# Kernel tuning notes

Measured on AMD Instinct MI355X. Metric: run time of the kernel, lower is better.

The kernel has to match this reference:

```python
import jax, jax.numpy as jnp
import numpy as np
from jax import lax

K_KNN = 20           # DGCNN default neighborhood size
SLOPE = 0.2          # LeakyReLU negative slope


def _leaky(x):
    return jnp.where(x >= 0, x, SLOPE * x)


def _knn(x, k):
    # x: [B, N, C] -> idx [B, N, k] of nearest neighbors (incl. self) in feature space
    xx = jnp.sum(x * x, axis=-1)                       # [B, N]
    d = xx[:, :, None] + xx[:, None, :] - 2.0 * jnp.einsum('bnc,bmc->bnm', x, x)
    return lax.top_k(-d, k)[1]                          # [B, N, k]


def _edge_conv(x, idx, w, b):
    # x: [B, N, C]; idx: [B, N, k]; w: [O, 2C]; b: [O]
    neigh = jax.vmap(lambda xt, i: xt[i])(x, idx)       # [B, N, k, C]
    center = jnp.broadcast_to(x[:, :, None, :], neigh.shape)
    feat = jnp.concatenate([neigh - center, center], axis=-1)  # [B, N, k, 2C]
    h = _leaky(jnp.einsum('bnkc,oc->bnko', feat, w) + b)
    return jnp.max(h, axis=2)                           # [B, N, O]


def setup_inputs() -> dict:
    key = jax.random.key(0)
    ks = jax.random.split(key, 20)
    B, N, J, KR = 4, 4096, 24, 4
    layers = [64, 128, 256]

    def w_init(k, o, i):
        return jax.random.normal(k, (o, i), jnp.float32) / np.sqrt(i)

    inp = {
        'V': jax.random.normal(ks[0], (B, N, 3), jnp.float32),
        'W': jax.random.uniform(ks[1], (B, J, N), jnp.float32),
        'skeletonOneRingIdx': jax.random.randint(ks[2], (B, J, KR), 0, J),
    }
    # geoNet edge-conv params (input channels per layer: 3, 64, 128 -> 2C inputs)
    inp['g1_w'] = w_init(ks[3], 64, 6);    inp['g1_b'] = jnp.zeros((64,), jnp.float32)
    inp['g2_w'] = w_init(ks[4], 128, 128); inp['g2_b'] = jnp.zeros((128,), jnp.float32)
    inp['g3_w'] = w_init(ks[5], 256, 256); inp['g3_b'] = jnp.zeros((256,), jnp.float32)
    # skeleton edge-conv params (inputs: 451 -> 902, 256 -> 512, 128 -> 256)
    inp['s1_w'] = w_init(ks[6], 256, 902); inp['s1_b'] = jnp.zeros((256,), jnp.float32)
    inp['s2_w'] = w_init(ks[7], 128, 512); inp['s2_b'] = jnp.zeros((128,), jnp.float32)
    inp['s3_w'] = w_init(ks[8], 64, 256);  inp['s3_b'] = jnp.zeros((64,), jnp.float32)
    # jointMLP 1x1 convs: 448 -> 512 -> 256 -> 3
    inp['m1_w'] = w_init(ks[9], 512, 448);  inp['m1_b'] = jnp.zeros((512,), jnp.float32)
    inp['m2_w'] = w_init(ks[10], 256, 512); inp['m2_b'] = jnp.zeros((256,), jnp.float32)
    inp['m3_w'] = w_init(ks[11], 3, 256);   inp['m3_b'] = jnp.zeros((3,), jnp.float32)
    return inp


def reference(V, W, skeletonOneRingIdx,
              g1_w, g1_b, g2_w, g2_b, g3_w, g3_b,
              s1_w, s1_b, s2_w, s2_b, s3_w, s3_b,
              m1_w, m1_b, m2_w, m2_b, m3_w, m3_b):
    # ---- geoNet: DGCNN with dynamic kNN, output cat([xyz, l1, l2, l3]) -> [B, N, 451]
    outs = [V]
    h = V
    for w, b in ((g1_w, g1_b), (g2_w, g2_b), (g3_w, g3_b)):
        idx = _knn(h, K_KNN)
        h = _edge_conv(h, idx, w, b)
        outs.append(h)
    feat = jnp.concatenate(outs, axis=-1)                # [B, N, 451]

    # ---- weighted pooling onto skeleton joints
    pooled = jnp.einsum('bjn,bnc->bjc', W, feat)
    pooled = pooled / (jnp.sum(W, axis=-1, keepdims=True) + 1e-5)  # [B, J, 451]

    # ---- skeleton edge convs with fixed one-ring idx
    v1 = _edge_conv(pooled, skeletonOneRingIdx, s1_w, s1_b)  # [B, J, 256]
    v2 = _edge_conv(v1, skeletonOneRingIdx, s2_w, s2_b)      # [B, J, 128]
    v3 = _edge_conv(v2, skeletonOneRingIdx, s3_w, s3_b)      # [B, J, 64]

    joints = jnp.concatenate([v1, v2, v3], axis=-1)          # [B, J, 448]
    h = _leaky(jnp.einsum('bjc,oc->bjo', joints, m1_w) + m1_b)
    h = _leaky(jnp.einsum('bjc,oc->bjo', h, m2_w) + m2_b)
    out = jnp.einsum('bjc,oc->bjo', h, m3_w) + m3_b          # [B, J, 3]
    return out
```

## Files before the change

kernel.cpp:

```cpp
#include <hip/hip_runtime.h>
#include <hip/hip_bf16.h>
#include <float.h>

#define B_   4
#define N_   4096
#define J_   24
#define KR_  4
#define KNN_ 20
#define SLOPE 0.2f
#define SLABN 64
#define NSLAB (N_ / SLABN)
#define NTILE 32
#define SCAP 768
#define KSLACK 8u

typedef __attribute__((ext_vector_type(8))) short bf16x8;
typedef __attribute__((ext_vector_type(4))) float f32x4;

__global__ void k_norm(const float* __restrict__ h, float* __restrict__ xx, int C) {
    int i = blockIdx.x * blockDim.x + threadIdx.x;
    if (i >= B_ * N_) return;
    const float* hp = h + (size_t)i * C;
    float s = 0.f;
    for (int c = 0; c < C; ++c) { float v = hp[c]; s += v * v; }
    xx[i] = s;
}

__device__ __forceinline__ unsigned mapf(float f) {
    unsigned u = __float_as_uint(f);
    return (u & 0x80000000u) ? ~u : (u | 0x80000000u);
}
__device__ __forceinline__ unsigned key16(float f) {
    return mapf(f) >> 16;
}

__global__ void k_split(const float* __restrict__ h, unsigned short* __restrict__ hi,
                        unsigned short* __restrict__ lo, int total4) {
    int i = blockIdx.x * 256 + threadIdx.x;
    if (i >= total4) return;
    float4 v = ((const float4*)h)[i];
    ushort4 h4, l4;
    {
        unsigned u = __float_as_uint(v.x); h4.x = (unsigned short)(u >> 16);
        float r = v.x - __uint_as_float(u & 0xffff0000u); l4.x = (unsigned short)(__float_as_uint(r) >> 16);
    }
    {
        unsigned u = __float_as_uint(v.y); h4.y = (unsigned short)(u >> 16);
        float r = v.y - __uint_as_float(u & 0xffff0000u); l4.y = (unsigned short)(__float_as_uint(r) >> 16);
    }
    {
        unsigned u = __float_as_uint(v.z); h4.z = (unsigned short)(u >> 16);
        float r = v.z - __uint_as_float(u & 0xffff0000u); l4.z = (unsigned short)(__float_as_uint(r) >> 16);
    }
    {
        unsigned u = __float_as_uint(v.w); h4.w = (unsigned short)(u >> 16);
        float r = v.w - __uint_as_float(u & 0xffff0000u); l4.w = (unsigned short)(__float_as_uint(r) >> 16);
    }
    ((ushort4*)hi)[i] = h4;
    ((ushort4*)lo)[i] = l4;
}

__global__ __launch_bounds__(256) void k_dist(const unsigned short* __restrict__ Hi,
                                              const unsigned short* __restrict__ Lo,
                                              int C,
                                              const float* __restrict__ xxall,
                                              unsigned short* __restrict__ Dall, int b0) {
    __shared__ unsigned short tile[128][136];
    int b = b0 + blockIdx.y;
    const unsigned short* XH = Hi + (size_t)b * N_ * C;
    const unsigned short* XL = Lo + (size_t)b * N_ * C;
    const float* xxb = xxall + (size_t)b * N_;
    unsigned short* D = Dall + (size_t)blockIdx.y * N_ * N_;

    int t = blockIdx.x;
    int ti = 0;
    while (t >= NTILE - ti) { t -= NTILE - ti; ++ti; }
    int tj = ti + t;
    int row0 = ti * 128, col0 = tj * 128;
    int tid  = threadIdx.x;
    int wv   = tid >> 6, lane = tid & 63;
    int wr   = wv >> 1,  wc   = wv & 1;
    int rbase = row0 + wr * 64;
    int cbase = col0 + wc * 64;
    int lp    = lane & 15;
    int kgrp  = lane >> 4;

    f32x4 acc[4][4];
#pragma unroll
    for (int i = 0; i < 4; ++i)
#pragma unroll
        for (int j = 0; j < 4; ++j) acc[i][j] = (f32x4){0.f, 0.f, 0.f, 0.f};

    for (int ks = 0; ks < C; ks += 32) {
        int kb = ks + kgrp * 8;
        bf16x8 ah[4], al[4];
#pragma unroll
        for (int fi = 0; fi < 4; ++fi) {
            size_t ro = (size_t)(rbase + fi * 16 + lp) * C + kb;
            ah[fi] = *(const bf16x8*)(XH + ro);
            al[fi] = *(const bf16x8*)(XL + ro);
        }
#pragma unroll
        for (int fj = 0; fj < 4; ++fj) {
            size_t co = (size_t)(cbase + fj * 16 + lp) * C + kb;
            bf16x8 bh = *(const bf16x8*)(XH + co);
            bf16x8 bl = *(const bf16x8*)(XL + co);
#pragma unroll
            for (int fi = 0; fi < 4; ++fi) {
                acc[fi][fj] = __builtin_amdgcn_mfma_f32_16x16x32_bf16(ah[fi], bh, acc[fi][fj], 0, 0, 0);
                acc[fi][fj] = __builtin_amdgcn_mfma_f32_16x16x32_bf16(ah[fi], bl, acc[fi][fj], 0, 0, 0);
                acc[fi][fj] = __builtin_amdgcn_mfma_f32_16x16x32_bf16(al[fi], bh, acc[fi][fj], 0, 0, 0);
            }
        }
    }

    float xxrv = xxb[rbase + lane];
    float xxcv = xxb[cbase + lane];
    int rsub = (lane >> 4) * 4;
#pragma unroll
    for (int fi = 0; fi < 4; ++fi) {
#pragma unroll
        for (int fj = 0; fj < 4; ++fj) {
            float xc = __shfl(xxcv, fj * 16 + lp, 64);
#pragma unroll
            for (int r = 0; r < 4; ++r) {
                float xr = __shfl(xxrv, fi * 16 + rsub + r, 64);
                float d = xr + xc - 2.f * acc[fi][fj][r];
                tile[wr * 64 + fi * 16 + rsub + r][wc * 64 + fj * 16 + lp] =
                    (unsigned short)key16(d);
            }
        }
    }
    __syncthreads();

    {
        int r0   = tid >> 4;
        int cseg = (tid & 15) * 8;
#pragma unroll
        for (int q = 0; q < 8; ++q) {
            int row = r0 + q * 16;
            *(uint4*)(D + (size_t)(row0 + row) * N_ + col0 + cseg) =
                *(const uint4*)&tile[row][cseg];
        }
    }
    if (ti == tj) return;
    {
        int c0g = tid >> 4;
        int g   = tid & 15;
#pragma unroll
        for (int cq = 0; cq < 8; ++cq) {
            int c = c0g + cq * 16;
            unsigned short s[8];
#pragma unroll
            for (int q = 0; q < 8; ++q) s[q] = tile[g * 8 + q][c];
            *(uint4*)(D + (size_t)(col0 + c) * N_ + row0 + g * 8) = *(const uint4*)s;
        }
    }
}

__device__ __forceinline__ unsigned long long shflx64(unsigned long long v, int m) {
    unsigned lo = (unsigned)v, hi = (unsigned)(v >> 32);
    lo = (unsigned)__shfl_xor((int)lo, m, 64);
    hi = (unsigned)__shfl_xor((int)hi, m, 64);
    return ((unsigned long long)hi << 32) | lo;
}

__device__ __forceinline__ float bsort64f(float v, int lane) {
#pragma unroll
    for (int k = 2; k <= 64; k <<= 1) {
#pragma unroll
        for (int j = k >> 1; j > 0; j >>= 1) {
            float o = __shfl_xor(v, j, 64);
            bool keepmin = (((lane & j) == 0) == ((lane & k) == 0));
            float mn = fminf(v, o), mx = fmaxf(v, o);
            v = keepmin ? mn : mx;
        }
    }
    return v;
}

__device__ __forceinline__ unsigned bsort64i(unsigned v, int lane) {
#pragma unroll
    for (int k = 2; k <= 64; k <<= 1) {
#pragma unroll
        for (int j = k >> 1; j > 0; j >>= 1) {
            unsigned o = (unsigned)__shfl_xor((int)v, j, 64);
            bool keepmin = (((lane & j) == 0) == ((lane & k) == 0));
            unsigned mn = (v < o) ? v : o;
            unsigned mx = (v < o) ? o : v;
            v = keepmin ? mn : mx;
        }
    }
    return v;
}

__device__ __forceinline__ unsigned long long bsort64u(unsigned long long v, int lane) {
#pragma unroll
    for (int k = 2; k <= 64; k <<= 1) {
#pragma unroll
        for (int j = k >> 1; j > 0; j >>= 1) {
            unsigned long long o = shflx64(v, j);
            bool keepmin = (((lane & j) == 0) == ((lane & k) == 0));
            bool oless = o < v;
            unsigned long long mn = oless ? o : v;
            unsigned long long mx = oless ? v : o;
            v = keepmin ? mn : mx;
        }
    }
    return v;
}

__global__ __launch_bounds__(256) void k_sel(const unsigned short* __restrict__ Dall,
                                             const float* __restrict__ Xall, int C,
                                             const float* __restrict__ xxall,
                                             int* __restrict__ knnIdx, int b0) {
    __shared__ unsigned sidx[SCAP];
    __shared__ unsigned long long skey[SCAP];
    __shared__ float qf[128];
    __shared__ unsigned stau[4];
    __shared__ int scnt;
    int b = b0 + blockIdx.y;
    const unsigned short* Db = Dall + (size_t)blockIdx.y * N_ * N_;
    const float* Xb  = Xall + (size_t)b * N_ * C;
    const float* xxb = xxall + (size_t)b * N_;
    int* idxout = knnIdx + (size_t)b * N_ * KNN_;
    int ql   = blockIdx.x;
    int wv   = threadIdx.x >> 6;
    int lane = threadIdx.x & 63;
    int gbase = wv * 1024 + lane * 16;
    if (threadIdx.x == 0) scnt = 0;
    for (int c = threadIdx.x; c < C; c += 256) qf[c] = Xb[(size_t)ql * C + c];

    const uint4* kp = (const uint4*)(Db + (size_t)ql * N_ + gbase);
    uint4 pa = kp[0], pb = kp[1];
    unsigned kv[16];
    kv[0] = pa.x & 0xffffu;  kv[1] = pa.x >> 16;
    kv[2] = pa.y & 0xffffu;  kv[3] = pa.y >> 16;
    kv[4] = pa.z & 0xffffu;  kv[5] = pa.z >> 16;
    kv[6] = pa.w & 0xffffu;  kv[7] = pa.w >> 16;
    kv[8] = pb.x & 0xffffu;  kv[9] = pb.x >> 16;
    kv[10] = pb.y & 0xffffu; kv[11] = pb.y >> 16;
    kv[12] = pb.z & 0xffffu; kv[13] = pb.z >> 16;
    kv[14] = pb.w & 0xffffu; kv[15] = pb.w >> 16;

    unsigned mn = kv[0];
#pragma unroll
    for (int t = 1; t < 16; ++t) mn = (kv[t] < mn) ? kv[t] : mn;
    mn = bsort64i(mn, lane);
    unsigned tw = (unsigned)__shfl((int)mn, 19, 64);
    if (lane == 0) stau[wv] = tw;
    __syncthreads();
    unsigned tau = stau[0];
    tau = (stau[1] < tau) ? stau[1] : tau;
    tau = (stau[2] < tau) ? stau[2] : tau;
    tau = (stau[3] < tau) ? stau[3] : tau;
    tau += KSLACK;
    if (tau > 0xffffu) tau = 0xffffu;

#pragma unroll
    for (int t = 0; t < 16; ++t) {
        if (kv[t] <= tau) {
            int p = atomicAdd(&scnt, 1);
            if (p < SCAP) sidx[p] = (unsigned)(gbase + t);
        }
    }
    __syncthreads();
    int S = scnt; if (S > SCAP) S = SCAP;
    float xxq = xxb[ql];
    const float4* xq4 = (const float4*)qf;
    for (int s = threadIdx.x; s < S; s += 256) {
        int j = (int)sidx[s];
        const float4* xj = (const float4*)(Xb + (size_t)j * C);
        float a0 = 0.f, a1 = 0.f, a2 = 0.f, a3 = 0.f;
        for (int c4 = 0; c4 < (C >> 2); ++c4) {
            float4 x = xj[c4]; float4 qv = xq4[c4];
            a0 = fmaf(qv.x, x.x, a0);
            a1 = fmaf(qv.y, x.y, a1);
            a2 = fmaf(qv.z, x.z, a2);
            a3 = fmaf(qv.w, x.w, a3);
        }
        float dot = (a0 + a1) + (a2 + a3);
        float d = xxq + xxb[j] - 2.f * dot;
        skey[s] = ((unsigned long long)mapf(d) << 32) | (unsigned)j;
    }
    __syncthreads();
    if (wv != 0) return;
    unsigned long long key = (lane < S) ? skey[lane] : ~0ull;
    key = bsort64u(key, lane);
    for (int consumed = 64; consumed < S; consumed += 44) {
        if (lane >= 20) {
            int src = consumed + lane - 20;
            key = (src < S) ? skey[src] : ~0ull;
        }
        key = bsort64u(key, lane);
    }
    if (lane < KNN_) idxout[ql * KNN_ + lane] = (int)(unsigned)key;
}

__global__ __launch_bounds__(256) void k_selC3(const float* __restrict__ V,
                                               const float* __restrict__ xx,
                                               int* __restrict__ knnIdx) {
    __shared__ unsigned long long sbuf[SCAP];
    __shared__ float stau[4];
    __shared__ int scnt;
    int b    = blockIdx.y;
    const float* Xb  = V + (size_t)b * N_ * 3;
    const float* xxb = xx + (size_t)b * N_;
    int* idxout = knnIdx + (size_t)b * N_ * KNN_;
    int q    = blockIdx.x;
    int wv   = threadIdx.x >> 6;
    int lane = threadIdx.x & 63;
    int gbase = wv * 1024 + lane * 16;
    if (threadIdx.x == 0) scnt = 0;

    float qx = Xb[q * 3], qy = Xb[q * 3 + 1], qz = Xb[q * 3 + 2];
    float xxq = xxb[q];

    float pts[48];
    const float4* src = (const float4*)(Xb + (size_t)gbase * 3);
#pragma unroll
    for (int t = 0; t < 12; ++t) ((float4*)pts)[t] = src[t];

    float dv[16];
#pragma unroll
    for (int t = 0; t < 16; ++t) {
        float dot = qx * pts[3 * t];
        dot = fmaf(qy, pts[3 * t + 1], dot);
        dot = fmaf(qz, pts[3 * t + 2], dot);
        dv[t] = xxq + xxb[gbase + t] - 2.f * dot;
    }

    float mn = dv[0];
#pragma unroll
    for (int t = 1; t < 16; ++t) mn = fminf(mn, dv[t]);
    mn = bsort64f(mn, lane);
    float tw = __shfl(mn, 19, 64);
    if (lane == 0) stau[wv] = tw;
    __syncthreads();
    float tau = fminf(fminf(stau[0], stau[1]), fminf(stau[2], stau[3]));

#pragma unroll
    for (int t = 0; t < 16; ++t) {
        if (dv[t] <= tau) {
            int p = atomicAdd(&scnt, 1);
            if (p < SCAP)
                sbuf[p] = ((unsigned long long)mapf(dv[t]) << 32) | (unsigned)(gbase + t);
        }
    }
    __syncthreads();
    if (wv != 0) return;
    int S = scnt; if (S > SCAP) S = SCAP;
    unsigned long long key = (lane < S) ? sbuf[lane] : ~0ull;
    key = bsort64u(key, lane);
    for (int consumed = 64; consumed < S; consumed += 44) {
        if (lane >= 20) {
            int srci = consumed + lane - 20;
            key = (srci < S) ? sbuf[srci] : ~0ull;
        }
        key = bsort64u(key, lane);
    }
    if (lane < KNN_) idxout[q * KNN_ + lane] = (int)(unsigned)key;
}

__device__ __forceinline__ void prepP_elem(const float* __restrict__ w,
                                           const float* __restrict__ bias,
                                           int C, int O, float* __restrict__ P,
                                           float* __restrict__ b2, int i) {
    int O2 = 2 * O;
    if (i < O2) b2[i] = (i < O) ? 0.f : bias[i - O];
    if (i >= C * O2) return;
    int k = i / O2, col = i % O2;
    float v;
    if (col < O) v = w[(size_t)col * 2 * C + k];
    else { int o = col - O; v = w[(size_t)o * 2 * C + C + k] - w[(size_t)o * 2 * C + k]; }
    P[i] = v;
}
__device__ __forceinline__ void transp_elem(const float* __restrict__ w, int O, int K,
                                            float* __restrict__ wT, int i) {
    if (i >= O * K) return;
    int k = i / O, o = i % O;
    wT[i] = w[(size_t)o * K + k];
}

__global__ void k_prepall(const float* g1w, const float* g1b,
                          const float* g2w, const float* g2b,
                          const float* g3w, const float* g3b,
                          const float* s1w, const float* s1b,
                          const float* s2w, const float* s2b,
                          const float* s3w, const float* s3b,
                          const float* m1w, const float* m2w, const float* m3w,
                          float* P1, float* P2, float* P3, float* P4, float* P5,
                          float* P6, float* P7, float* P8, float* P9,
                          float* bb1, float* bb2, float* bb3,
                          float* bb4, float* bb5, float* bb6) {
    int i = blockIdx.x * 256 + threadIdx.x;
    switch (blockIdx.y) {
        case 0: prepP_elem(g1w, g1b, 3,   64,  P1, bb1, i); break;
        case 1: prepP_elem(g2w, g2b, 64,  128, P2, bb2, i); break;
        case 2: prepP_elem(g3w, g3b, 128, 256, P3, bb3, i); break;
        case 3: prepP_elem(s1w, s1b, 451, 256, P4, bb4, i); break;
        case 4: prepP_elem(s2w, s2b, 256, 128, P5, bb5, i); break;
        case 5: prepP_elem(s3w, s3b, 128, 64,  P6, bb6, i); break;
        case 6: transp_elem(m1w, 512, 448, P7, i); break;
        case 7: transp_elem(m2w, 256, 512, P8, i); break;
        case 8: transp_elem(m3w, 3,   256, P9, i); break;
    }
}

__global__ __launch_bounds__(256) void k_gemm(const float* __restrict__ A, int lda,
                                              const float* __restrict__ Bm,
                                              float* __restrict__ Cm, int ldc,
                                              int M, int N, int K,
                                              const float* __restrict__ bias, int leaky) {
    __shared__ float As[16][68];
    __shared__ float Bs[16][68];
    int tid = threadIdx.x;
    int row0 = blockIdx.y * 64, col0 = blockIdx.x * 64;
    int tr = tid >> 4, tc = tid & 15;
    float acc[4][4] = {{0.f}};
    for (int kt = 0; kt < K; kt += 16) {
#pragma unroll
        for (int i = 0; i < 4; ++i) {
            int e = tid + 256 * i;
            int r = e >> 4, kk = e & 15;
            int gr = row0 + r, gk = kt + kk;
            float v = 0.f;
            if (gr < M && gk < K) v = A[(size_t)gr * lda + gk];
            As[kk][r] = v;
        }
#pragma unroll
        for (int i = 0; i < 4; ++i) {
            int e = tid + 256 * i;
            int kk = e >> 6, c = e & 63;
            int gk = kt + kk, gc = col0 + c;
            float v = 0.f;
            if (gk < K && gc < N) v = Bm[(size_t)gk * N + gc];
            Bs[kk][c] = v;
        }
        __syncthreads();
#pragma unroll
        for (int kk = 0; kk < 16; ++kk) {
            float a[4], bv[4];
            *(float4*)&a[0]  = *(const float4*)&As[kk][tr * 4];
            *(float4*)&bv[0] = *(const float4*)&Bs[kk][tc * 4];
#pragma unroll
            for (int i = 0; i < 4; ++i)
#pragma unroll
                for (int j = 0; j < 4; ++j) acc[i][j] += a[i] * bv[j];
        }
        __syncthreads();
    }
#pragma unroll
    for (int i = 0; i < 4; ++i) {
        int r = row0 + tr * 4 + i;
        if (r >= M) continue;
#pragma unroll
        for (int j = 0; j < 4; ++j) {
            int c = col0 + tc * 4 + j;
            if (c >= N) continue;
            float v = acc[i][j];
            if (bias) v += bias[c];
            if (leaky) v = v >= 0.f ? v : SLOPE * v;
            Cm[(size_t)r * ldc + c] = v;
        }
    }
}

__global__ __launch_bounds__(256) void k_sgemm(const float* __restrict__ A, int lda,
                                               const float* __restrict__ Bm,
                                               float* __restrict__ Cm, int ldc,
                                               int N, int K,
                                               const float* __restrict__ bias, int leaky) {
    extern __shared__ float Arow[];
    int r   = blockIdx.x;
    int c0  = blockIdx.y * 256;
    int tid = threadIdx.x;
    for (int k = tid; k < K; k += 256) Arow[k] = A[(size_t)r * lda + k];
    __syncthreads();
    int c = c0 + tid;
    if (c >= N) return;
    float acc = bias ? bias[c] : 0.f;
    for (int k = 0; k < K; ++k) acc += Arow[k] * Bm[(size_t)k * N + c];
    if (leaky) acc = acc >= 0.f ? acc : SLOPE * acc;
    Cm[(size_t)r * ldc + c] = acc;
}

__global__ void k_gathermax(const float* __restrict__ Y, int O, int R,
                            const int* __restrict__ idx, int kc,
                            float* __restrict__ out, int ldo, int ooff,
                            float* __restrict__ xxout) {
    extern __shared__ int sidx[];
    __shared__ float red[256];
    int br = blockIdx.x;
    int b  = br / R;
    int o  = threadIdx.x;
    if (o < kc) sidx[o] = idx[(size_t)br * kc + o];
    __syncthreads();
    int O2 = 2 * O;
    float z = Y[(size_t)br * O2 + O + o];
    float best = -FLT_MAX;
    for (int k = 0; k < kc; ++k) {
        int m = sidx[k];
        best = fmaxf(best, Y[(size_t)(b * R + m) * O2 + o]);
    }
    float r = z + best;
    r = r >= 0.f ? r : SLOPE * r;
    out[(size_t)br * ldo + ooff + o] = r;
    if (xxout) {
        red[o] = r * r;
        __syncthreads();
        for (int s = blockDim.x >> 1; s > 0; s >>= 1) {
            if (o < s) red[o] += red[o + s];
            __syncthreads();
        }
        if (o == 0) xxout[br] = red[0];
    }
}

__device__ __forceinline__ void chan_map(int b, int c,
                                         const float* Vf, const float* l1,
                                         const float* l2, const float* l3,
                                         const float*& p, int& st) {
    if (c < 3)        { st = 3;   p = Vf + (size_t)b * N_ * 3   + c; }
    else if (c < 67)  { st = 64;  p = l1 + (size_t)b * N_ * 64  + (c - 3); }
    else if (c < 195) { st = 128; p = l2 + (size_t)b * N_ * 128 + (c - 67); }
    else              { st = 256; p = l3 + (size_t)b * N_ * 256 + (c - 195); }
}

__global__ __launch_bounds__(256) void k_pool2(const float* __restrict__ Vf,
                                               const float* __restrict__ l1,
                                               const float* __restrict__ l2,
                                               const float* __restrict__ l3,
                                               const float* __restrict__ W,
                                               float* __restrict__ ppool,
                                               float* __restrict__ psw) {
    __shared__ float Wl[SLABN][J_];
    int blk  = blockIdx.x;
    int b    = blk / NSLAB, slab = blk % NSLAB;
    int n0   = slab * SLABN;
    int tid  = threadIdx.x;

    for (int e = tid; e < J_ * SLABN; e += 256) {
        int j = e / SLABN, n = e % SLABN;
        Wl[n][j] = W[((size_t)b * J_ + j) * N_ + n0 + n];
    }
    __syncthreads();

    if (tid < J_) {
        float s = 0.f;
        for (int n = 0; n < SLABN; ++n) s += Wl[n][tid];
        psw[(size_t)blk * J_ + tid] = s;
    }

    int c0 = tid, c1 = tid + 256;
    const float *p0, *p1 = nullptr; int s0, s1 = 0;
    chan_map(b, c0, Vf, l1, l2, l3, p0, s0);
    bool has1 = (c1 < 451);
    if (has1) chan_map(b, c1, Vf, l1, l2, l3, p1, s1);

    float acc0[J_], acc1[J_];
#pragma unroll
    for (int j = 0; j < J_; ++j) { acc0[j] = 0.f; acc1[j] = 0.f; }

    for (int n = 0; n < SLABN; ++n) {
        float v0 = p0[(size_t)(n0 + n) * s0];
        float v1 = has1 ? p1[(size_t)(n0 + n) * s1] : 0.f;
        const float* wn = &Wl[n][0];
#pragma unroll
        for (int q = 0; q < J_ / 4; ++q) {
            float4 w4 = *(const float4*)(wn + 4 * q);
            acc0[4*q+0] += w4.x * v0;  acc1[4*q+0] += w4.x * v1;
            acc0[4*q+1] += w4.y * v0;  acc1[4*q+1] += w4.y * v1;
            acc0[4*q+2] += w4.z * v0;  acc1[4*q+2] += w4.z * v1;
            acc0[4*q+3] += w4.w * v0;  acc1[4*q+3] += w4.w * v1;
        }
    }
    float* pp = ppool + (size_t)blk * J_ * 451;
#pragma unroll
    for (int j = 0; j < J_; ++j) {
        pp[(size_t)j * 451 + c0] = acc0[j];
        if (has1) pp[(size_t)j * 451 + c1] = acc1[j];
    }
}

__global__ __launch_bounds__(256) void k_poolred(const float* __restrict__ ppool,
                                                 const float* __restrict__ psw,
                                                 float* __restrict__ pooled) {
    int bj = blockIdx.x;
    int b  = bj / J_, j = bj % J_;
    int tid = threadIdx.x;

    float sw = 0.f;
    for (int sl = 0; sl < NSLAB; ++sl) sw += psw[(size_t)(b * NSLAB + sl) * J_ + j];
    float inv = 1.f / (sw + 1e-5f);

    for (int c = tid; c < 451; c += 256) {
        float s = 0.f;
        for (int sl = 0; sl < NSLAB; ++sl)
            s += ppool[((size_t)(b * NSLAB + sl) * J_ + j) * 451 + c];
        pooled[(size_t)bj * 451 + c] = s * inv;
    }
}

extern "C" void kernel_launch(void* const* d_in, const int* in_sizes, int n_in,
                              void* d_out, int out_size, void* d_ws, size_t ws_size,
                              hipStream_t stream) {
    const float* V  = (const float*)d_in[0];
    const float* W  = (const float*)d_in[1];
    const int* ringIdx = (const int*)d_in[2];
    const float* g1w = (const float*)d_in[3];
    const float* g1b = (const float*)d_in[4];
    const float* g2w = (const float*)d_in[5];
    const float* g2b = (const float*)d_in[6];
    const float* g3w = (const float*)d_in[7];
    const float* g3b = (const float*)d_in[8];
    const float* s1w = (const float*)d_in[9];
    const float* s1b = (const float*)d_in[10];
    const float* s2w = (const float*)d_in[11];
    const float* s2b = (const float*)d_in[12];
    const float* s3w = (const float*)d_in[13];
    const float* s3b = (const float*)d_in[14];
    const float* m1w = (const float*)d_in[15];
    const float* m1b = (const float*)d_in[16];
    const float* m2w = (const float*)d_in[17];
    const float* m2b = (const float*)d_in[18];
    const float* m3w = (const float*)d_in[19];
    const float* m3b = (const float*)d_in[20];
    (void)n_in; (void)in_sizes; (void)out_size;

    const int szP1 = 3 * 128,    szP2 = 64 * 256,  szP3 = 128 * 512;
    const int szP4 = 451 * 512,  szP5 = 256 * 256, szP6 = 128 * 128;
    const int szP7 = 448 * 512,  szP8 = 512 * 256, szP9 = 256 * 3;

    auto dreg_floats = [&](int nd) -> size_t {
        size_t a = (size_t)nd * ((size_t)N_ * N_ / 2);
        size_t ymax = (size_t)B_ * N_ * 512;
        size_t pool = (size_t)B_ * NSLAB * J_ * 451 + (size_t)B_ * NSLAB * J_;
        size_t r = a;
        if (ymax > r) r = ymax;
        if (pool > r) r = pool;
        return r;
    };
    auto layout_bytes = [&](int nd) -> size_t {
        size_t f = 0;
        f += (size_t)B_ * N_ * 64 + (size_t)B_ * N_ * 128 + (size_t)B_ * N_ * 256;
        f += (size_t)B_ * N_;
        f += dreg_floats(nd);
        f += 2 * ((size_t)B_ * N_ * 128 / 2);
        f += (size_t)B_ * N_ * KNN_;
        f += (size_t)B_ * J_ * 451 + (size_t)B_ * J_ * 448;
        f += (size_t)B_ * J_ * 512 + (size_t)B_ * J_ * 256;
        f += (size_t)(szP1 + szP2 + szP3 + szP4 + szP5 + szP6 + szP7 + szP8 + szP9);
        f += 128 + 256 + 512 + 512 + 256 + 128;
        return f * 4;
    };
    int nb = 1;
    if (ws_size >= layout_bytes(4)) nb = 4;
    else if (ws_size >= layout_bytes(2)) nb = 2;

    float* ws = (float*)d_ws;
    size_t off = 0;
    float* l1 = ws + off; off += (size_t)B_ * N_ * 64;
    float* l2 = ws + off; off += (size_t)B_ * N_ * 128;
    float* l3 = ws + off; off += (size_t)B_ * N_ * 256;
    float* xx = ws + off; off += (size_t)B_ * N_;
    float* D  = ws + off; off += dreg_floats(nb);
    unsigned short* Dk = (unsigned short*)D;
    float* Y  = D;
    float* ppool = D;
    float* psw   = D + (size_t)B_ * NSLAB * J_ * 451;
    unsigned short* Xhi = (unsigned short*)(ws + off); off += (size_t)B_ * N_ * 128 / 2;
    unsigned short* Xlo = (unsigned short*)(ws + off); off += (size_t)B_ * N_ * 128 / 2;
    int* knnIdx = (int*)(ws + off); off += (size_t)B_ * N_ * KNN_;
    float* pooled = ws + off; off += (size_t)B_ * J_ * 451;
    float* joints = ws + off; off += (size_t)B_ * J_ * 448;
    float* h1 = ws + off; off += (size_t)B_ * J_ * 512;
    float* h2 = ws + off; off += (size_t)B_ * J_ * 256;
    float* P1 = ws + off; off += szP1;
    float* P2 = ws + off; off += szP2;
    float* P3 = ws + off; off += szP3;
    float* P4 = ws + off; off += szP4;
    float* P5 = ws + off; off += szP5;
    float* P6 = ws + off; off += szP6;
    float* P7 = ws + off; off += szP7;
    float* P8 = ws + off; off += szP8;
    float* P9 = ws + off; off += szP9;
    float* bb1 = ws + off; off += 128;
    float* bb2 = ws + off; off += 256;
    float* bb3 = ws + off; off += 512;
    float* bb4 = ws + off; off += 512;
    float* bb5 = ws + off; off += 256;
    float* bb6 = ws + off; off += 128;

    const int M = B_ * N_;
    const int MJ = B_ * J_;
    const int NUTRI = NTILE * (NTILE + 1) / 2;

    k_prepall<<<dim3((szP4 + 255) / 256, 9), 256, 0, stream>>>(
        g1w, g1b, g2w, g2b, g3w, g3b, s1w, s1b, s2w, s2b, s3w, s3b,
        m1w, m2w, m3w, P1, P2, P3, P4, P5, P6, P7, P8, P9,
        bb1, bb2, bb3, bb4, bb5, bb6);

    k_norm<<<(M + 255) / 256, 256, 0, stream>>>(V, xx, 3);
    k_selC3<<<dim3(N_, B_), 256, 0, stream>>>(V, xx, knnIdx);
    k_gemm<<<dim3(2, M / 64), 256, 0, stream>>>(V, 3, P1, Y, 128, M, 128, 3, bb1, 0);
    k_gathermax<<<M, 64, KNN_ * sizeof(int), stream>>>(Y, 64, N_, knnIdx, KNN_, l1, 64, 0, xx);

    k_split<<<(M * 64 / 4 + 255) / 256, 256, 0, stream>>>(l1, Xhi, Xlo, M * 64 / 4);
    for (int g = 0; g < B_; g += nb) {
        k_dist<<<dim3(NUTRI, nb), 256, 0, stream>>>(Xhi, Xlo, 64, xx, Dk, g);
        k_sel<<<dim3(N_, nb), 256, 0, stream>>>(Dk, l1, 64, xx, knnIdx, g);
    }
    k_gemm<<<dim3(4, M / 64), 256, 0, stream>>>(l1, 64, P2, Y, 256, M, 256, 64, bb2, 0);
    k_gathermax<<<M, 128, KNN_ * sizeof(int), stream>>>(Y, 128, N_, knnIdx, KNN_, l2, 128, 0, xx);

    k_split<<<(M * 128 / 4 + 255) / 256, 256, 0, stream>>>(l2, Xhi, Xlo, M * 128 / 4);
    for (int g = 0; g < B_; g += nb) {
        k_dist<<<dim3(NUTRI, nb), 256, 0, stream>>>(Xhi, Xlo, 128, xx, Dk, g);
        k_sel<<<dim3(N_, nb), 256, 0, stream>>>(Dk, l2, 128, xx, knnIdx, g);
    }
    k_gemm<<<dim3(8, M / 64), 256, 0, stream>>>(l2, 128, P3, Y, 512, M, 512, 128, bb3, 0);
    k_gathermax<<<M, 256, KNN_ * sizeof(int), stream>>>(Y, 256, N_, knnIdx, KNN_, l3, 256, 0, nullptr);

    k_pool2<<<B_ * NSLAB, 256, 0, stream>>>(V, l1, l2, l3, W, ppool, psw);
    k_poolred<<<MJ, 256, 0, stream>>>(ppool, psw, pooled);

    k_sgemm<<<dim3(MJ, 2), 256, 451 * sizeof(float), stream>>>(pooled, 451, P4, Y, 512, 512, 451, bb4, 0);
    k_gathermax<<<MJ, 256, KR_ * sizeof(int), stream>>>(Y, 256, J_, ringIdx, KR_, joints, 448, 0, nullptr);

    k_sgemm<<<dim3(MJ, 1), 256, 256 * sizeof(float), stream>>>(joints, 448, P5, Y, 256, 256, 256, bb5, 0);
    k_gathermax<<<MJ, 128, KR_ * sizeof(int), stream>>>(Y, 128, J_, ringIdx, KR_, joints, 448, 256, nullptr);

    k_sgemm<<<dim3(MJ, 1), 256, 128 * sizeof(float), stream>>>(joints + 256, 448, P6, Y, 128, 128, 128, bb6, 0);
    k_gathermax<<<MJ, 64, KR_ * sizeof(int), stream>>>(Y, 64, J_, ringIdx, KR_, joints, 448, 384, nullptr);

    k_sgemm<<<dim3(MJ, 2), 256, 448 * sizeof(float), stream>>>(joints, 448, P7, h1, 512, 512, 448, m1b, 1);
    k_sgemm<<<dim3(MJ, 1), 256, 512 * sizeof(float), stream>>>(h1, 512, P8, h2, 256, 256, 512, m2b, 1);
    k_sgemm<<<dim3(MJ, 1), 256, 256 * sizeof(float), stream>>>(h2, 256, P9, (float*)d_out, 3, 3, 256, m3b, 0);
}
```

Before: 890.5 us.

## Replace bitonic-sort kNN selection with ballot-based radix select

Swaps the full 64-lane bitonic sorts used to find the per-wave threshold and the final top-20 for a ballot/popcount radix-select. The threshold now needs one ballot per key bit instead of 21 shuffle/compare stages. The final merge keeps only the current winners and refills the rest of the wave from the candidate buffer, then ranks the winners with a small shared-memory count. The aim is to cut shuffle and sort work in the selection kernels. The trade-off is more serial ballot loops (32 plus 12 bits per round) and extra subtle tie-handling logic, since only the low 12 index bits are used.

Result: slower. 961.1 us (+7.9%).

```diff
diff --git a/kernel.cpp b/kernel.cpp
--- a/kernel.cpp
+++ b/kernel.cpp
@@ -158,56 +158,69 @@
     }
 }
 
-__device__ __forceinline__ unsigned long long shflx64(unsigned long long v, int m) {
-    unsigned lo = (unsigned)v, hi = (unsigned)(v >> 32);
-    lo = (unsigned)__shfl_xor((int)lo, m, 64);
-    hi = (unsigned)__shfl_xor((int)hi, m, 64);
-    return ((unsigned long long)hi << 32) | lo;
-}
-
-__device__ __forceinline__ float bsort64f(float v, int lane) {
-#pragma unroll
-    for (int k = 2; k <= 64; k <<= 1) {
-#pragma unroll
-        for (int j = k >> 1; j > 0; j >>= 1) {
-            float o = __shfl_xor(v, j, 64);
-            bool keepmin = (((lane & j) == 0) == ((lane & k) == 0));
-            float mn = fminf(v, o), mx = fmaxf(v, o);
-            v = keepmin ? mn : mx;
-        }
-    }
-    return v;
-}
-
-__device__ __forceinline__ unsigned bsort64i(unsigned v, int lane) {
-#pragma unroll
-    for (int k = 2; k <= 64; k <<= 1) {
-#pragma unroll
-        for (int j = k >> 1; j > 0; j >>= 1) {
-            unsigned o = (unsigned)__shfl_xor((int)v, j, 64);
-            bool keepmin = (((lane & j) == 0) == ((lane & k) == 0));
-            unsigned mn = (v < o) ? v : o;
-            unsigned mx = (v < o) ? o : v;
-            v = keepmin ? mn : mx;
-        }
-    }
-    return v;
-}
-
-__device__ __forceinline__ unsigned long long bsort64u(unsigned long long v, int lane) {
-#pragma unroll
-    for (int k = 2; k <= 64; k <<= 1) {
-#pragma unroll
-        for (int j = k >> 1; j > 0; j >>= 1) {
-            unsigned long long o = shflx64(v, j);
-            bool keepmin = (((lane & j) == 0) == ((lane & k) == 0));
-            bool oless = o < v;
-            unsigned long long mn = oless ? o : v;
-            unsigned long long mx = oless ? v : o;
-            v = keepmin ? mn : mx;
-        }
-    }
-    return v;
+__device__ __forceinline__ unsigned radixsel_wave(unsigned val, int r, int nbits) {
+    unsigned long long cand = ~0ull;
+    unsigned prefix = 0;
+    for (int bit = nbits - 1; bit >= 0; --bit) {
+        unsigned long long z = cand & __ballot(!((val >> bit) & 1u));
+        int cz = __popcll(z);
+        if (cz >= r) cand = z;
+        else { r -= cz; cand &= ~z; prefix |= 1u << bit; }
+    }
+    return prefix;
+}
+
+__device__ __forceinline__ bool top20_round(unsigned long long key, bool active) {
+    unsigned hi = (unsigned)(key >> 32);
+    unsigned lo = (unsigned)key;
+    unsigned long long amask = __ballot(active);
+    int navail = __popcll(amask);
+    if (navail <= KNN_) return active;
+    int r = KNN_;
+    unsigned long long cand = amask;
+    unsigned prefix = 0;
+    for (int bit = 31; bit >= 0; --bit) {
+        unsigned long long z = cand & __ballot(!((hi >> bit) & 1u));
+        int cz = __popcll(z);
+        if (cz >= r) cand = z;
+        else { r -= cz; cand &= ~z; prefix |= 1u << bit; }
+    }
+    unsigned long long c2 = __ballot(active && hi == prefix);
+    unsigned p2 = 0;
+    for (int bit = 11; bit >= 0; --bit) {
+        unsigned long long z = c2 & __ballot(!((lo >> bit) & 1u));
+        int cz = __popcll(z);
+        if (cz >= r) c2 = z;
+        else { r -= cz; c2 &= ~z; p2 |= 1u << bit; }
+    }
+    return active && (hi < prefix || (hi == prefix && lo <= p2));
+}
+
+__device__ __forceinline__ void final_top20(const unsigned long long* skey, int S,
+                                            unsigned long long* wbuf,
+                                            int lane, int* idxout, int obase) {
+    unsigned long long key = (lane < S) ? skey[lane] : ~0ull;
+    bool active = (lane < S) && (lane < 64);
+    int consumed = (S < 64) ? S : 64;
+    int nw = 0;
+    for (;;) {
+        bool win = top20_round(key, active);
+        unsigned long long wb = __ballot(win);
+        nw = __popcll(wb);
+        int pos = __popcll(wb & ((1ull << lane) - 1ull));
+        if (win) wbuf[pos] = key;
+        if (consumed >= S) break;
+        int src = consumed + lane - nw;
+        key = (lane < nw) ? wbuf[lane] : ((src < S) ? skey[src] : ~0ull);
+        active = (lane < nw) || (src >= consumed && src < S);
+        consumed += 64 - nw;
+    }
+    if (lane < nw) {
+        unsigned long long mine = wbuf[lane];
+        int rank = 0;
+        for (int i = 0; i < nw; ++i) rank += (wbuf[i] < mine);
+        idxout[obase + rank] = (int)(unsigned)mine;
+    }
 }
 
 __global__ __launch_bounds__(256) void k_sel(const unsigned short* __restrict__ Dall,
@@ -216,6 +229,7 @@
                                              int* __restrict__ knnIdx, int b0) {
     __shared__ unsigned sidx[SCAP];
     __shared__ unsigned long long skey[SCAP];
+    __shared__ unsigned long long wbuf[24];
     __shared__ float qf[128];
     __shared__ unsigned stau[4];
     __shared__ int scnt;
@@ -225,11 +239,12 @@
     const float* xxb = xxall + (size_t)b * N_;
     int* idxout = knnIdx + (size_t)b * N_ * KNN_;
     int ql   = blockIdx.x;
-    int wv   = threadIdx.x >> 6;
-    int lane = threadIdx.x & 63;
+    int tid  = threadIdx.x;
+    int wv   = tid >> 6;
+    int lane = tid & 63;
     int gbase = wv * 1024 + lane * 16;
-    if (threadIdx.x == 0) scnt = 0;
-    for (int c = threadIdx.x; c < C; c += 256) qf[c] = Xb[(size_t)ql * C + c];
+    if (tid == 0) scnt = 0;
+    for (int c = tid; c < C; c += 256) qf[c] = Xb[(size_t)ql * C + c];
 
     const uint4* kp = (const uint4*)(Db + (size_t)ql * N_ + gbase);
     uint4 pa = kp[0], pb = kp[1];
@@ -246,9 +261,8 @@
     unsigned mn = kv[0];
 #pragma unroll
     for (int t = 1; t < 16; ++t) mn = (kv[t] < mn) ? kv[t] : mn;
-    mn = bsort64i(mn, lane);
-    unsigned tw = (unsigned)__shfl((int)mn, 19, 64);
-    if (lane == 0) stau[wv] = tw;
+    unsigned Bw = radixsel_wave(mn, KNN_, 16);
+    if (lane == 0) stau[wv] = Bw;
     __syncthreads();
     unsigned tau = stau[0];
     tau = (stau[1] < tau) ? stau[1] : tau;
@@ -268,7 +282,7 @@
     int S = scnt; if (S > SCAP) S = SCAP;
     float xxq = xxb[ql];
     const float4* xq4 = (const float4*)qf;
-    for (int s = threadIdx.x; s < S; s += 256) {
+    for (int s = tid; s < S; s += 256) {
         int j = (int)sidx[s];
         const float4* xj = (const float4*)(Xb + (size_t)j * C);
         float a0 = 0.f, a1 = 0.f, a2 = 0.f, a3 = 0.f;
@@ -285,33 +299,26 @@
     }
     __syncthreads();
     if (wv != 0) return;
-    unsigned long long key = (lane < S) ? skey[lane] : ~0ull;
-    key = bsort64u(key, lane);
-    for (int consumed = 64; consumed < S; consumed += 44) {
-        if (lane >= 20) {
-            int src = consumed + lane - 20;
-            key = (src < S) ? skey[src] : ~0ull;
-        }
-        key = bsort64u(key, lane);
-    }
-    if (lane < KNN_) idxout[ql * KNN_ + lane] = (int)(unsigned)key;
+    final_top20(skey, S, wbuf, lane, idxout, ql * KNN_);
 }
 
 __global__ __launch_bounds__(256) void k_selC3(const float* __restrict__ V,
                                                const float* __restrict__ xx,
                                                int* __restrict__ knnIdx) {
     __shared__ unsigned long long sbuf[SCAP];
-    __shared__ float stau[4];
+    __shared__ unsigned long long wbuf[24];
+    __shared__ unsigned stau[4];
     __shared__ int scnt;
     int b    = blockIdx.y;
     const float* Xb  = V + (size_t)b * N_ * 3;
     const float* xxb = xx + (size_t)b * N_;
     int* idxout = knnIdx + (size_t)b * N_ * KNN_;
     int q    = blockIdx.x;
-    int wv   = threadIdx.x >> 6;
-    int lane = threadIdx.x & 63;
+    int tid  = threadIdx.x;
+    int wv   = tid >> 6;
+    int lane = tid & 63;
     int gbase = wv * 1024 + lane * 16;
-    if (threadIdx.x == 0) scnt = 0;
+    if (tid == 0) scnt = 0;
 
     float qx = Xb[q * 3], qy = Xb[q * 3 + 1], qz = Xb[q * 3 + 2];
     float xxq = xxb[q];
@@ -321,45 +328,39 @@
 #pragma unroll
     for (int t = 0; t < 12; ++t) ((float4*)pts)[t] = src[t];
 
-    float dv[16];
+    unsigned kk[16];
 #pragma unroll
     for (int t = 0; t < 16; ++t) {
         float dot = qx * pts[3 * t];
         dot = fmaf(qy, pts[3 * t + 1], dot);
         dot = fmaf(qz, pts[3 * t + 2], dot);
-        dv[t] = xxq + xxb[gbase + t] - 2.f * dot;
-    }
-
-    float mn = dv[0];
-#pragma unroll
-    for (int t = 1; t < 16; ++t) mn = fminf(mn, dv[t]);
-    mn = bsort64f(mn, lane);
-    float tw = __shfl(mn, 19, 64);
-    if (lane == 0) stau[wv] = tw;
-    __syncthreads();
-    float tau = fminf(fminf(stau[0], stau[1]), fminf(stau[2], stau[3]));
+        float d = xxq + xxb[gbase + t] - 2.f * dot;
+        kk[t] = mapf(d);
+    }
+
+    unsigned mn = kk[0];
+#pragma unroll
+    for (int t = 1; t < 16; ++t) mn = (kk[t] < mn) ? kk[t] : mn;
+    unsigned Bw = radixsel_wave(mn, KNN_, 32);
+    if (lane == 0) stau[wv] = Bw;
+    __syncthreads();
+    unsigned tau = stau[0];
+    tau = (stau[1] < tau) ? stau[1] : tau;
+    tau = (stau[2] < tau) ? stau[2] : tau;
+    tau = (stau[3] < tau) ? stau[3] : tau;
 
 #pragma unroll
     for (int t = 0; t < 16; ++t) {
-        if (dv[t] <= tau) {
+        if (kk[t] <= tau) {
             int p = atomicAdd(&scnt, 1);
             if (p < SCAP)
-                sbuf[p] = ((unsigned long long)mapf(dv[t]) << 32) | (unsigned)(gbase + t);
+                sbuf[p] = ((unsigned long long)kk[t] << 32) | (unsigned)(gbase + t);
         }
     }
     __syncthreads();
     if (wv != 0) return;
     int S = scnt; if (S > SCAP) S = SCAP;
-    unsigned long long key = (lane < S) ? sbuf[lane] : ~0ull;
-    key = bsort64u(key, lane);
-    for (int consumed = 64; consumed < S; consumed += 44) {
-        if (lane >= 20) {
-            int srci = consumed + lane - 20;
-            key = (srci < S) ? sbuf[srci] : ~0ull;
-        }
-        key = bsort64u(key, lane);
-    }
-    if (lane < KNN_) idxout[q * KNN_ + lane] = (int)(unsigned)key;
+    final_top20(sbuf, S, wbuf, lane, idxout, q * KNN_);
 }
 
 __device__ __forceinline__ void prepP_elem(const float* __restrict__ w,
```
